# Optimization experiments

Measured on AMD Instinct MI355X. Metric: run time of the kernel, lower is better.

## Reference

```python
import jax, jax.numpy as jnp
import numpy as np

NUM_HEADS = 16
DIM_EMBED = 1024
DIM_K = DIM_EMBED // NUM_HEADS


def setup_inputs() -> dict:
    key = jax.random.key(0)
    ks = jax.random.split(key, 11)
    B, S, D = 2, 2048, DIM_EMBED
    scale = 1.0 / np.sqrt(D)
    inp = {
        "query": jax.random.normal(ks[0], (B, S, D), dtype=jnp.float32),
        "key": jax.random.normal(ks[1], (B, S, D), dtype=jnp.float32),
        "value": jax.random.normal(ks[2], (B, S, D), dtype=jnp.float32),
        # torch nn.Linear weights: [out_features, in_features], y = x @ W.T + b
        "Wq": jax.random.normal(ks[3], (D, D), dtype=jnp.float32) * scale,
        "bq": jnp.zeros((D,), dtype=jnp.float32),
        "Wk": jax.random.normal(ks[4], (D, D), dtype=jnp.float32) * scale,
        "bk": jnp.zeros((D,), dtype=jnp.float32),
        "Wv": jax.random.normal(ks[5], (D, D), dtype=jnp.float32) * scale,
        "bv": jnp.zeros((D,), dtype=jnp.float32),
        "Wo": jax.random.normal(ks[6], (D, D), dtype=jnp.float32) * scale,
        "bo": jnp.zeros((D,), dtype=jnp.float32),
    }
    return inp


def _split_heads(x):
    B, S, D = x.shape
    return x.reshape(B, S, NUM_HEADS, DIM_K).transpose(0, 2, 1, 3)  # [B,H,S,dk]


def reference(query, key, value, Wq, bq, Wk, bk, Wv, bv, Wo, bo):
    q = _split_heads(query @ Wq.T + bq)   # [B,H,S,dk]
    k = _split_heads(key @ Wk.T + bk)
    v = _split_heads(value @ Wv.T + bv)
    # reactivity = q @ k^T, scaled AFTER matmul as in the original
    reactivity = jnp.einsum("bhsd,bhtd->bhst", q, k)
    attention_score = jax.nn.softmax(reactivity / np.sqrt(DIM_K), axis=-1)
    blended = jnp.einsum("bhst,bhtd->bhsd", attention_score, v)  # [B,H,S,dk]
    B, H, S, dk = blended.shape
    blended = blended.transpose(0, 2, 1, 3).reshape(B, S, H * dk)
    out = blended @ Wo.T + bo
    return out, attention_score
```

## Files before the change

kernel.cpp:

```cpp
#include <hip/hip_runtime.h>
#include <stdint.h>

#define BATCH 2
#define SEQ   2048
#define DEMB  1024
#define NHEAD 16
#define DK    64
#define NTOK  (BATCH * SEQ)
#define OUT_ELEMS ((size_t)NTOK * DEMB)

typedef __bf16 bf16x8 __attribute__((ext_vector_type(8)));
typedef float  f32x4  __attribute__((ext_vector_type(4)));
union FragU { uint4 u; bf16x8 b; };

__device__ __forceinline__ unsigned short f2bf(float f) {
  union { float f; unsigned u; } v; v.f = f;
  unsigned r = v.u + 0x7fffu + ((v.u >> 16) & 1u);
  return (unsigned short)(r >> 16);
}

__device__ __forceinline__ void gll16(const void* g, void* l) {
  __builtin_amdgcn_global_load_lds(
      (const __attribute__((address_space(1))) void*)g,
      (__attribute__((address_space(3))) void*)l, 16, 0, 0);
}

__global__ __launch_bounds__(256) void k_cvt(
    const float* __restrict__ q, const float* __restrict__ k, const float* __restrict__ v,
    const float* __restrict__ wq, const float* __restrict__ wk,
    const float* __restrict__ wv, const float* __restrict__ wo,
    unsigned short* __restrict__ dq, unsigned short* __restrict__ dk,
    unsigned short* __restrict__ dv, unsigned short* __restrict__ dwq,
    unsigned short* __restrict__ dwk, unsigned short* __restrict__ dwv,
    unsigned short* __restrict__ dwo)
{
  const int t = blockIdx.y;
  const float* s; unsigned short* d; int n4;
  switch (t) {
    case 0: s = q;  d = dq;  n4 = NTOK * DEMB / 4; break;
    case 1: s = k;  d = dk;  n4 = NTOK * DEMB / 4; break;
    case 2: s = v;  d = dv;  n4 = NTOK * DEMB / 4; break;
    case 3: s = wq; d = dwq; n4 = DEMB * DEMB / 4; break;
    case 4: s = wk; d = dwk; n4 = DEMB * DEMB / 4; break;
    case 5: s = wv; d = dwv; n4 = DEMB * DEMB / 4; break;
    default: s = wo; d = dwo; n4 = DEMB * DEMB / 4; break;
  }
  for (int i = blockIdx.x * 256 + threadIdx.x; i < n4; i += gridDim.x * 256) {
    float4 f = ((const float4*)s)[i];
    ushort4 o; o.x = f2bf(f.x); o.y = f2bf(f.y); o.z = f2bf(f.z); o.w = f2bf(f.w);
    ((ushort4*)d)[i] = o;
  }
}

__global__ __launch_bounds__(256) void k_proj(
    const unsigned short* __restrict__ Xqb, const unsigned short* __restrict__ Xkb,
    const unsigned short* __restrict__ Xvb,
    const unsigned short* __restrict__ Wqb, const unsigned short* __restrict__ Wkb,
    const unsigned short* __restrict__ Wvb,
    const float* __restrict__ bq, const float* __restrict__ bk, const float* __restrict__ bv,
    unsigned short* __restrict__ qh, unsigned short* __restrict__ kh,
    unsigned short* __restrict__ vh)
{
  const int p = blockIdx.z;
  const unsigned short* __restrict__ X = (p == 0) ? Xqb : (p == 1) ? Xkb : Xvb;
  const unsigned short* __restrict__ W = (p == 0) ? Wqb : (p == 1) ? Wkb : Wvb;
  const float* __restrict__ bias       = (p == 0) ? bq  : (p == 1) ? bk  : bv;
  unsigned short* __restrict__ dst     = (p == 0) ? qh  : (p == 1) ? kh  : vh;

  __shared__ unsigned short As[128][64];
  __shared__ unsigned short Bs[128][64];

  const int tid  = threadIdx.x;
  const int lane = tid & 63;
  const int w    = tid >> 6;
  const int wm   = (w & 1) * 64;
  const int wn   = (w >> 1) * 64;
  const int l15  = lane & 15;
  const int quad = lane >> 4;

  const int o0  = blockIdx.x * 128;
  const int t0b = blockIdx.y * 128;

  f32x4 acc[4][4];
#pragma unroll
  for (int mi = 0; mi < 4; ++mi)
#pragma unroll
    for (int ni = 0; ni < 4; ++ni) acc[mi][ni] = {0.f, 0.f, 0.f, 0.f};

  for (int kk = 0; kk < DEMB; kk += 64) {
#pragma unroll
    for (int r = 0; r < 4; ++r) {
      int idx = tid + r * 256;
      int row = idx >> 3, c = (idx & 7) * 8;
      gll16(&W[(size_t)(o0 + row) * DEMB + kk + c], (unsigned short*)As + idx * 8);
      gll16(&X[(size_t)(t0b + row) * DEMB + kk + c], (unsigned short*)Bs + idx * 8);
    }
    __syncthreads();
#pragma unroll
    for (int k0 = 0; k0 < 64; k0 += 32) {
      FragU af[4], bfr[4];
#pragma unroll
      for (int mi = 0; mi < 4; ++mi)
        af[mi].u = *(const uint4*)&As[wm + mi * 16 + l15][k0 + quad * 8];
#pragma unroll
      for (int ni = 0; ni < 4; ++ni)
        bfr[ni].u = *(const uint4*)&Bs[wn + ni * 16 + l15][k0 + quad * 8];
#pragma unroll
      for (int mi = 0; mi < 4; ++mi)
#pragma unroll
        for (int ni = 0; ni < 4; ++ni)
          acc[mi][ni] = __builtin_amdgcn_mfma_f32_16x16x32_bf16(af[mi].b, bfr[ni].b, acc[mi][ni], 0, 0, 0);
    }
    __syncthreads();
  }

#pragma unroll
  for (int mi = 0; mi < 4; ++mi) {
    const int ob = o0 + wm + mi * 16 + quad * 4;
    const float4 bi = *(const float4*)&bias[ob];
    const int h_ = ob >> 6, db = ob & 63;
#pragma unroll
    for (int ni = 0; ni < 4; ++ni) {
      int token = t0b + wn + ni * 16 + l15;
      int b_ = token >> 11, s_ = token & 2047;
      ushort4 ov;
      ov.x = f2bf(acc[mi][ni][0] + bi.x);
      ov.y = f2bf(acc[mi][ni][1] + bi.y);
      ov.z = f2bf(acc[mi][ni][2] + bi.z);
      ov.w = f2bf(acc[mi][ni][3] + bi.w);
      *(ushort4*)&dst[(((size_t)b_ * NHEAD + h_) * SEQ + s_) * DK + db] = ov;
    }
  }
}

__global__ __launch_bounds__(256) void k_vt(const unsigned short* __restrict__ vh,
                                            unsigned short* __restrict__ vt)
{
  const int bh = blockIdx.y, s0 = blockIdx.x * 64;
  const size_t hoff = (size_t)bh * SEQ * DK;
  __shared__ unsigned short Ls[64][72];
  const int tid = threadIdx.x;
#pragma unroll
  for (int r = 0; r < 2; ++r) {
    int idx = tid + r * 256, row = idx >> 3, c = (idx & 7) * 8;
    uint4 v = *(const uint4*)&vh[hoff + (size_t)(s0 + row) * DK + c];
    *(uint4*)&Ls[row][c] = v;
  }
  __syncthreads();
#pragma unroll
  for (int r = 0; r < 2; ++r) {
    int idx = tid + r * 256, d = idx >> 3, c = (idx & 7) * 8;
    unsigned short tmp[8];
#pragma unroll
    for (int j = 0; j < 8; ++j) tmp[j] = Ls[c + j][d];
    *(uint4*)&vt[hoff + (size_t)d * SEQ + s0 + c] = *(const uint4*)tmp;
  }
}

__global__ __launch_bounds__(256, 4) void k_attn(
    const unsigned short* __restrict__ qh, const unsigned short* __restrict__ kh,
    const unsigned short* __restrict__ vt, unsigned short* __restrict__ blended,
    float* __restrict__ Pout)
{
  const int bh = blockIdx.y;
  const int s0 = blockIdx.x * 64;
  const size_t hoff = (size_t)bh * SEQ * DK;

  __shared__ unsigned short Ps[2][64][64];
  __shared__ float rowpart[4][64];
  __shared__ float recipS[64];

  const int tid  = threadIdx.x;
  const int lane = tid & 63;
  const int w    = tid >> 6;
  const int l15  = lane & 15;
  const int quad = lane >> 4;

  FragU qf[4][2];
#pragma unroll
  for (int mi = 0; mi < 4; ++mi)
#pragma unroll
    for (int k0 = 0; k0 < 2; ++k0)
      qf[mi][k0].u = *(const uint4*)&qh[hoff + (size_t)(s0 + mi * 16 + l15) * DK + k0 * 32 + quad * 8];

  const unsigned short* kbase = kh + hoff + (size_t)(w * 16 + l15) * DK + quad * 8;
  const unsigned short* vbase = vt + hoff + (size_t)(w * 16 + l15) * SEQ + quad * 8;

  float rs[4] = {0.f, 0.f, 0.f, 0.f};
#pragma unroll 2
  for (int t0 = 0; t0 < SEQ; t0 += 64) {
    FragU kf0, kf1;
    kf0.u = *(const uint4*)(kbase + (size_t)t0 * DK);
    kf1.u = *(const uint4*)(kbase + (size_t)t0 * DK + 32);
#pragma unroll
    for (int mi = 0; mi < 4; ++mi) {
      f32x4 a = {0.f, 0.f, 0.f, 0.f};
      a = __builtin_amdgcn_mfma_f32_16x16x32_bf16(kf0.b, qf[mi][0].b, a, 0, 0, 0);
      a = __builtin_amdgcn_mfma_f32_16x16x32_bf16(kf1.b, qf[mi][1].b, a, 0, 0, 0);
      rs[mi] += __expf(a[0] * 0.125f) + __expf(a[1] * 0.125f)
              + __expf(a[2] * 0.125f) + __expf(a[3] * 0.125f);
    }
  }
#pragma unroll
  for (int mi = 0; mi < 4; ++mi) {
    float v = rs[mi];
    v += __shfl_xor(v, 16); v += __shfl_xor(v, 32);
    rs[mi] = v;
  }
  if (lane < 16) {
#pragma unroll
    for (int mi = 0; mi < 4; ++mi) rowpart[w][mi * 16 + lane] = rs[mi];
  }
  __syncthreads();
  if (tid < 64)
    recipS[tid] = 1.0f / (rowpart[0][tid] + rowpart[1][tid] + rowpart[2][tid] + rowpart[3][tid]);
  __syncthreads();
  float rcp[4];
#pragma unroll
  for (int mi = 0; mi < 4; ++mi) rcp[mi] = recipS[mi * 16 + l15];

  f32x4 accpv[4];
#pragma unroll
  for (int mi = 0; mi < 4; ++mi) accpv[mi] = {0.f, 0.f, 0.f, 0.f};

  for (int t0 = 0, buf = 0; t0 < SEQ; t0 += 64, buf ^= 1) {
    FragU kf0, kf1, vf0, vf1;
    kf0.u = *(const uint4*)(kbase + (size_t)t0 * DK);
    kf1.u = *(const uint4*)(kbase + (size_t)t0 * DK + 32);
    vf0.u = *(const uint4*)(vbase + t0);
    vf1.u = *(const uint4*)(vbase + t0 + 32);
    unsigned short* Pb = &Ps[buf][0][0];
#pragma unroll
    for (int mi = 0; mi < 4; ++mi) {
      f32x4 a = {0.f, 0.f, 0.f, 0.f};
      a = __builtin_amdgcn_mfma_f32_16x16x32_bf16(kf0.b, qf[mi][0].b, a, 0, 0, 0);
      a = __builtin_amdgcn_mfma_f32_16x16x32_bf16(kf1.b, qf[mi][1].b, a, 0, 0, 0);
      float e0 = __expf(a[0] * 0.125f) * rcp[mi];
      float e1 = __expf(a[1] * 0.125f) * rcp[mi];
      float e2 = __expf(a[2] * 0.125f) * rcp[mi];
      float e3 = __expf(a[3] * 0.125f) * rcp[mi];
      float4 p4; p4.x = e0; p4.y = e1; p4.z = e2; p4.w = e3;
      *(float4*)&Pout[((size_t)bh * SEQ + s0 + mi * 16 + l15) * SEQ + t0 + w * 16 + quad * 4] = p4;
      ushort4 pb; pb.x = f2bf(e0); pb.y = f2bf(e1); pb.z = f2bf(e2); pb.w = f2bf(e3);
      const int row = mi * 16 + l15;
      const int u   = w * 4 + quad;
      *(ushort4*)(Pb + row * 64 + ((((u >> 1) ^ (row & 7)) << 3) | ((u & 1) << 2))) = pb;
    }
    __syncthreads();
#pragma unroll
    for (int mi = 0; mi < 4; ++mi) {
      const int row = mi * 16 + l15;
      FragU pf0, pf1;
      pf0.u = *(const uint4*)(Pb + row * 64 + ((quad ^ (row & 7)) << 3));
      pf1.u = *(const uint4*)(Pb + row * 64 + (((4 + quad) ^ (row & 7)) << 3));
      accpv[mi] = __builtin_amdgcn_mfma_f32_16x16x32_bf16(vf0.b, pf0.b, accpv[mi], 0, 0, 0);
      accpv[mi] = __builtin_amdgcn_mfma_f32_16x16x32_bf16(vf1.b, pf1.b, accpv[mi], 0, 0, 0);
    }
  }

  const int b_ = bh >> 4, h_ = bh & 15;
#pragma unroll
  for (int mi = 0; mi < 4; ++mi) {
    ushort4 ob;
    ob.x = f2bf(accpv[mi][0]); ob.y = f2bf(accpv[mi][1]);
    ob.z = f2bf(accpv[mi][2]); ob.w = f2bf(accpv[mi][3]);
    int token = b_ * SEQ + s0 + mi * 16 + l15;
    *(ushort4*)&blended[(size_t)token * DEMB + h_ * DK + w * 16 + quad * 4] = ob;
  }
}

__global__ __launch_bounds__(256) void k_outproj(
    const unsigned short* __restrict__ Wob, const unsigned short* __restrict__ blended,
    const float* __restrict__ bo, float* __restrict__ out)
{
  __shared__ unsigned short As[128][64];
  __shared__ unsigned short Bs[128][64];

  const int tid  = threadIdx.x;
  const int lane = tid & 63;
  const int w    = tid >> 6;
  const int wm   = (w & 1) * 64;
  const int wn   = (w >> 1) * 64;
  const int l15  = lane & 15;
  const int quad = lane >> 4;

  const int o0  = blockIdx.x * 128;
  const int t0b = blockIdx.y * 128;

  f32x4 acc[4][4];
#pragma unroll
  for (int mi = 0; mi < 4; ++mi)
#pragma unroll
    for (int ni = 0; ni < 4; ++ni) acc[mi][ni] = {0.f, 0.f, 0.f, 0.f};

  for (int kk = 0; kk < DEMB; kk += 64) {
#pragma unroll
    for (int r = 0; r < 4; ++r) {
      int idx = tid + r * 256;
      int row = idx >> 3, c = (idx & 7) * 8;
      gll16(&Wob[(size_t)(o0 + row) * DEMB + kk + c], (unsigned short*)As + idx * 8);
      gll16(&blended[(size_t)(t0b + row) * DEMB + kk + c], (unsigned short*)Bs + idx * 8);
    }
    __syncthreads();
#pragma unroll
    for (int k0 = 0; k0 < 64; k0 += 32) {
      FragU af[4], bfr[4];
#pragma unroll
      for (int mi = 0; mi < 4; ++mi)
        af[mi].u = *(const uint4*)&As[wm + mi * 16 + l15][k0 + quad * 8];
#pragma unroll
      for (int ni = 0; ni < 4; ++ni)
        bfr[ni].u = *(const uint4*)&Bs[wn + ni * 16 + l15][k0 + quad * 8];
#pragma unroll
      for (int mi = 0; mi < 4; ++mi)
#pragma unroll
        for (int ni = 0; ni < 4; ++ni)
          acc[mi][ni] = __builtin_amdgcn_mfma_f32_16x16x32_bf16(af[mi].b, bfr[ni].b, acc[mi][ni], 0, 0, 0);
    }
    __syncthreads();
  }

#pragma unroll
  for (int mi = 0; mi < 4; ++mi) {
    const int ob = o0 + wm + mi * 16 + quad * 4;
    const float4 bi = *(const float4*)&bo[ob];
#pragma unroll
    for (int ni = 0; ni < 4; ++ni) {
      int token = t0b + wn + ni * 16 + l15;
      float4 ov;
      ov.x = acc[mi][ni][0] + bi.x;
      ov.y = acc[mi][ni][1] + bi.y;
      ov.z = acc[mi][ni][2] + bi.z;
      ov.w = acc[mi][ni][3] + bi.w;
      *(float4*)&out[(size_t)token * DEMB + ob] = ov;
    }
  }
}

extern "C" void kernel_launch(void* const* d_in, const int* in_sizes, int n_in,
                              void* d_out, int out_size, void* d_ws, size_t ws_size,
                              hipStream_t stream) {
  const float* Xq = (const float*)d_in[0];
  const float* Xk = (const float*)d_in[1];
  const float* Xv = (const float*)d_in[2];
  const float* Wq = (const float*)d_in[3];
  const float* bq = (const float*)d_in[4];
  const float* Wk = (const float*)d_in[5];
  const float* bk = (const float*)d_in[6];
  const float* Wv = (const float*)d_in[7];
  const float* bv = (const float*)d_in[8];
  const float* Wo = (const float*)d_in[9];
  const float* bo = (const float*)d_in[10];

  float* out  = (float*)d_out;
  float* Pout = out + OUT_ELEMS;

  unsigned short* Xqb = (unsigned short*)d_ws;
  unsigned short* Xkb = Xqb + OUT_ELEMS;
  unsigned short* Xvb = Xkb + OUT_ELEMS;
  unsigned short* Wqb = Xvb + OUT_ELEMS;
  unsigned short* Wkb = Wqb + (size_t)DEMB * DEMB;
  unsigned short* Wvb = Wkb + (size_t)DEMB * DEMB;
  unsigned short* Wob = Wvb + (size_t)DEMB * DEMB;
  unsigned short* qh      = Wob + (size_t)DEMB * DEMB;
  unsigned short* kh      = qh + OUT_ELEMS;
  unsigned short* vh      = kh + OUT_ELEMS;
  unsigned short* vt      = vh + OUT_ELEMS;
  unsigned short* blended = vt + OUT_ELEMS;

  k_cvt<<<dim3(1024, 7), 256, 0, stream>>>(Xq, Xk, Xv, Wq, Wk, Wv, Wo,
                                           Xqb, Xkb, Xvb, Wqb, Wkb, Wvb, Wob);
  k_proj<<<dim3(8, 32, 3), 256, 0, stream>>>(Xqb, Xkb, Xvb, Wqb, Wkb, Wvb,
                                             bq, bk, bv, qh, kh, vh);
  k_vt<<<dim3(32, 32), 256, 0, stream>>>(vh, vt);
  k_attn<<<dim3(SEQ / 64, BATCH * NHEAD), 256, 0, stream>>>(qh, kh, vt, blended, Pout);
  k_outproj<<<dim3(8, 32), 256, 0, stream>>>(Wob, blended, bo, out);
}
```

Before: 833.8 us.

## Stage K and V tiles through double-buffered LDS with async global-to-LDS loads

The attention kernel now loads K and V^T tiles into swizzled, double-buffered shared memory using global_load_lds prefetch of the next tile, instead of each wave reading fragments straight from global memory. It synchronises with hand-written waitcnt/barrier asm and drops the double buffer on P in favour of a single buffer that it also reuses for the row-sum scratch. Occupancy is lowered to 3 blocks per SM to make room for the larger shared-memory footprint. The aim is to hide global load latency and share K/V tile loads across waves. The cost is extra barriers per tile and reduced occupancy, with a risk of ordering hazards from the manual vmcnt counts.

```diff
diff --git a/kernel.cpp b/kernel.cpp
--- a/kernel.cpp
+++ b/kernel.cpp
@@ -24,6 +24,10 @@
       (const __attribute__((address_space(1))) void*)g,
       (__attribute__((address_space(3))) void*)l, 16, 0, 0);
 }
+
+#define BAR_VM0()  asm volatile("s_waitcnt vmcnt(0) lgkmcnt(0)\n\ts_barrier" ::: "memory")
+#define BAR_LGKM() asm volatile("s_waitcnt lgkmcnt(0)\n\ts_barrier" ::: "memory")
+#define BAR_VM4()  asm volatile("s_waitcnt vmcnt(4) lgkmcnt(0)\n\ts_barrier" ::: "memory")
 
 __global__ __launch_bounds__(256) void k_cvt(
     const float* __restrict__ q, const float* __restrict__ k, const float* __restrict__ v,
@@ -157,7 +161,7 @@
   }
 }
 
-__global__ __launch_bounds__(256, 4) void k_attn(
+__global__ __launch_bounds__(256, 3) void k_attn(
     const unsigned short* __restrict__ qh, const unsigned short* __restrict__ kh,
     const unsigned short* __restrict__ vt, unsigned short* __restrict__ blended,
     float* __restrict__ Pout)
@@ -166,15 +170,22 @@
   const int s0 = blockIdx.x * 64;
   const size_t hoff = (size_t)bh * SEQ * DK;
 
-  __shared__ unsigned short Ps[2][64][64];
-  __shared__ float rowpart[4][64];
-  __shared__ float recipS[64];
+  __shared__ unsigned short Ks[2][64][64];
+  __shared__ unsigned short Vs[2][64][64];
+  __shared__ unsigned short Ps[64][64];
+  float* rowpart = (float*)&Ps[0][0];
+  float* recipS  = rowpart + 256;
 
   const int tid  = threadIdx.x;
   const int lane = tid & 63;
   const int w    = tid >> 6;
   const int l15  = lane & 15;
   const int quad = lane >> 4;
+  const int rx   = l15 & 7;
+
+  const int p0 = tid, p1 = tid + 256;
+  const int r0 = p0 >> 3, c0 = ((p0 & 7) ^ (r0 & 7)) * 8;
+  const int r1 = p1 >> 3, c1 = ((p1 & 7) ^ (r1 & 7)) * 8;
 
   FragU qf[4][2];
 #pragma unroll
@@ -183,15 +194,22 @@
     for (int k0 = 0; k0 < 2; ++k0)
       qf[mi][k0].u = *(const uint4*)&qh[hoff + (size_t)(s0 + mi * 16 + l15) * DK + k0 * 32 + quad * 8];
 
-  const unsigned short* kbase = kh + hoff + (size_t)(w * 16 + l15) * DK + quad * 8;
-  const unsigned short* vbase = vt + hoff + (size_t)(w * 16 + l15) * SEQ + quad * 8;
+  const int rr = w * 16 + l15;
+  const int fc0 = (quad ^ rx) * 8;
+  const int fc1 = ((quad + 4) ^ rx) * 8;
 
   float rs[4] = {0.f, 0.f, 0.f, 0.f};
-#pragma unroll 2
-  for (int t0 = 0; t0 < SEQ; t0 += 64) {
+  gll16(&kh[hoff + (size_t)r0 * DK + c0], (unsigned short*)Ks[0] + p0 * 8);
+  gll16(&kh[hoff + (size_t)r1 * DK + c1], (unsigned short*)Ks[0] + p1 * 8);
+  BAR_VM0();
+  for (int i = 0; i < 32; ++i) {
+    const int b = i & 1;
+    const size_t tn = (size_t)(((i + 1) & 31) * 64);
+    gll16(&kh[hoff + (tn + r0) * DK + c0], (unsigned short*)Ks[b ^ 1] + p0 * 8);
+    gll16(&kh[hoff + (tn + r1) * DK + c1], (unsigned short*)Ks[b ^ 1] + p1 * 8);
     FragU kf0, kf1;
-    kf0.u = *(const uint4*)(kbase + (size_t)t0 * DK);
-    kf1.u = *(const uint4*)(kbase + (size_t)t0 * DK + 32);
+    kf0.u = *(const uint4*)&Ks[b][rr][fc0];
+    kf1.u = *(const uint4*)&Ks[b][rr][fc1];
 #pragma unroll
     for (int mi = 0; mi < 4; ++mi) {
       f32x4 a = {0.f, 0.f, 0.f, 0.f};
@@ -200,6 +218,7 @@
       rs[mi] += __expf(a[0] * 0.125f) + __expf(a[1] * 0.125f)
               + __expf(a[2] * 0.125f) + __expf(a[3] * 0.125f);
     }
+    BAR_VM0();
   }
 #pragma unroll
   for (int mi = 0; mi < 4; ++mi) {
@@ -209,11 +228,11 @@
   }
   if (lane < 16) {
 #pragma unroll
-    for (int mi = 0; mi < 4; ++mi) rowpart[w][mi * 16 + lane] = rs[mi];
+    for (int mi = 0; mi < 4; ++mi) rowpart[w * 64 + mi * 16 + lane] = rs[mi];
   }
   __syncthreads();
   if (tid < 64)
-    recipS[tid] = 1.0f / (rowpart[0][tid] + rowpart[1][tid] + rowpart[2][tid] + rowpart[3][tid]);
+    recipS[tid] = 1.0f / (rowpart[tid] + rowpart[64 + tid] + rowpart[128 + tid] + rowpart[192 + tid]);
   __syncthreads();
   float rcp[4];
 #pragma unroll
@@ -223,13 +242,30 @@
 #pragma unroll
   for (int mi = 0; mi < 4; ++mi) accpv[mi] = {0.f, 0.f, 0.f, 0.f};
 
-  for (int t0 = 0, buf = 0; t0 < SEQ; t0 += 64, buf ^= 1) {
+  gll16(&kh[hoff + (size_t)r0 * DK + c0], (unsigned short*)Ks[0] + p0 * 8);
+  gll16(&kh[hoff + (size_t)r1 * DK + c1], (unsigned short*)Ks[0] + p1 * 8);
+  gll16(&vt[hoff + (size_t)r0 * SEQ + c0], (unsigned short*)Vs[0] + p0 * 8);
+  gll16(&vt[hoff + (size_t)r1 * SEQ + c1], (unsigned short*)Vs[0] + p1 * 8);
+  BAR_VM0();
+
+  const int u   = w * 4 + quad;
+  const int psw = (((u >> 1) ^ rx) << 3) | ((u & 1) << 2);
+  const int pr0 = (quad ^ rx) << 3;
+  const int pr1 = ((quad + 4) ^ rx) << 3;
+
+  for (int i = 0; i < 32; ++i) {
+    const int b  = i & 1;
+    const int t0 = i * 64;
+    const size_t tn = (size_t)(((i + 1) & 31) * 64);
+    gll16(&kh[hoff + (tn + r0) * DK + c0], (unsigned short*)Ks[b ^ 1] + p0 * 8);
+    gll16(&kh[hoff + (tn + r1) * DK + c1], (unsigned short*)Ks[b ^ 1] + p1 * 8);
+    gll16(&vt[hoff + (size_t)r0 * SEQ + tn + c0], (unsigned short*)Vs[b ^ 1] + p0 * 8);
+    gll16(&vt[hoff + (size_t)r1 * SEQ + tn + c1], (unsigned short*)Vs[b ^ 1] + p1 * 8);
     FragU kf0, kf1, vf0, vf1;
-    kf0.u = *(const uint4*)(kbase + (size_t)t0 * DK);
-    kf1.u = *(const uint4*)(kbase + (size_t)t0 * DK + 32);
-    vf0.u = *(const uint4*)(vbase + t0);
-    vf1.u = *(const uint4*)(vbase + t0 + 32);
-    unsigned short* Pb = &Ps[buf][0][0];
+    kf0.u = *(const uint4*)&Ks[b][rr][fc0];
+    kf1.u = *(const uint4*)&Ks[b][rr][fc1];
+    vf0.u = *(const uint4*)&Vs[b][rr][fc0];
+    vf1.u = *(const uint4*)&Vs[b][rr][fc1];
 #pragma unroll
     for (int mi = 0; mi < 4; ++mi) {
       f32x4 a = {0.f, 0.f, 0.f, 0.f};
@@ -242,20 +278,18 @@
       float4 p4; p4.x = e0; p4.y = e1; p4.z = e2; p4.w = e3;
       *(float4*)&Pout[((size_t)bh * SEQ + s0 + mi * 16 + l15) * SEQ + t0 + w * 16 + quad * 4] = p4;
       ushort4 pb; pb.x = f2bf(e0); pb.y = f2bf(e1); pb.z = f2bf(e2); pb.w = f2bf(e3);
-      const int row = mi * 16 + l15;
-      const int u   = w * 4 + quad;
-      *(ushort4*)(Pb + row * 64 + ((((u >> 1) ^ (row & 7)) << 3) | ((u & 1) << 2))) = pb;
-    }
-    __syncthreads();
+      *(ushort4*)((unsigned short*)&Ps[mi * 16 + l15][0] + psw) = pb;
+    }
+    BAR_LGKM();
 #pragma unroll
     for (int mi = 0; mi < 4; ++mi) {
-      const int row = mi * 16 + l15;
       FragU pf0, pf1;
-      pf0.u = *(const uint4*)(Pb + row * 64 + ((quad ^ (row & 7)) << 3));
-      pf1.u = *(const uint4*)(Pb + row * 64 + (((4 + quad) ^ (row & 7)) << 3));
+      pf0.u = *(const uint4*)((const unsigned short*)&Ps[mi * 16 + l15][0] + pr0);
+      pf1.u = *(const uint4*)((const unsigned short*)&Ps[mi * 16 + l15][0] + pr1);
       accpv[mi] = __builtin_amdgcn_mfma_f32_16x16x32_bf16(vf0.b, pf0.b, accpv[mi], 0, 0, 0);
       accpv[mi] = __builtin_amdgcn_mfma_f32_16x16x32_bf16(vf1.b, pf1.b, accpv[mi], 0, 0, 0);
     }
+    BAR_VM4();
   }
 
   const int b_ = bh >> 4, h_ = bh & 15;
```

New measurement: 814.6 us. 1.02x faster.
